# Kernel optimization log

Hardware: AMD Instinct MI355X
Metric: run time of the kernel (lower is better)

The kernel has to match this reference:

```python
import jax, jax.numpy as jnp
import numpy as np
import math

WIN = 2
TOPK = 3
GH, GW = 4, 4  # gabor splatting grid == upsampled window size


def _window_partition(img, ws):
    # img: (B, C, H, W) -> (B, num_windows, ws*ws, C)
    B, C, H, W = img.shape
    x = img.transpose(0, 2, 3, 1)  # B,H,W,C
    x = x.reshape(B, H // ws, ws, W // ws, ws, C)
    x = x.transpose(0, 1, 3, 2, 4, 5).reshape(B, -1, ws * ws, C)
    return x


def _gabor_map(theta, sigma, lam, psi, gamma):
    # build num 4x4 Gabor kernels from per-component params -> (num, GH, GW)
    cy = jnp.arange(GH, dtype=jnp.float32) - (GH - 1) / 2.0
    cx = jnp.arange(GW, dtype=jnp.float32) - (GW - 1) / 2.0
    yy, xx = jnp.meshgrid(cy, cx, indexing='ij')  # (GH, GW)
    th = theta[:, None, None] * (2.0 * jnp.pi)
    xp = xx[None] * jnp.cos(th) + yy[None] * jnp.sin(th)
    yp = -xx[None] * jnp.sin(th) + yy[None] * jnp.cos(th)
    sig = sigma[:, None, None] + 0.5  # keep positive
    lmb = lam[:, None, None] + 0.5
    gam = gamma[:, None, None]
    env = jnp.exp(-(xp ** 2 + (gam ** 2) * yp ** 2) / (2.0 * sig ** 2))
    carrier = jnp.cos(2.0 * jnp.pi * xp / lmb + psi[:, None, None])
    return env * carrier  # (num, GH, GW)


def setup_inputs() -> dict:
    key = jax.random.key(0)
    ks = jax.random.split(key, 8)
    B, Nt, Ns, C = 64, 64, 4096, 256
    return {
        'z': jax.random.normal(ks[0], (B, Nt, C), dtype=jnp.float32),
        'x': jax.random.normal(ks[1], (B, Ns, C), dtype=jnp.float32),
        'gabor_theta': jax.random.uniform(ks[2], (16,), dtype=jnp.float32),
        'gabor_sigma': jax.random.uniform(ks[3], (16,), dtype=jnp.float32),
        'gabor_lam': jax.random.uniform(ks[4], (16,), dtype=jnp.float32),
        'gabor_psi': jax.random.uniform(ks[5], (16,), dtype=jnp.float32),
        'gabor_gamma': jax.random.uniform(ks[6], (16,), dtype=jnp.float32),
        'gabor_weight': jax.random.normal(ks[7], (16,), dtype=jnp.float32),
    }


def reference(z, x, gabor_theta, gabor_sigma, gabor_lam, gabor_psi,
              gabor_gamma, gabor_weight):
    B, Nt, C = z.shape
    ht = int(math.isqrt(Nt))
    _, Ns, _ = x.shape
    hs = int(math.isqrt(Ns))

    z_img = z.transpose(0, 2, 1).reshape(B, C, ht, ht)
    z_max = z_img.max(axis=(2, 3))  # AdaptiveMaxPool2d((1,1)) -> (B, C)

    x_img = x.transpose(0, 2, 1).reshape(B, C, hs, hs)
    x_windows = _window_partition(x_img, WIN)

    # grouped 1x1 xcorr == per-pixel dot product with template vector
    response = jnp.einsum('bchw,bc->bhw', x_img, z_max)[:, None]  # (B,1,hs,hs)
    r_windows = _window_partition(response, WIN)
    win_mean = r_windows.mean(axis=2)[..., 0]  # (B, nW)

    _, idx = jax.lax.top_k(win_mean, TOPK)  # (B, TOPK)
    x_sel = jnp.take_along_axis(x_windows, idx[:, :, None, None], axis=1)
    x_win = x_sel.reshape(B, TOPK, WIN, WIN, C).transpose(0, 1, 4, 2, 3)
    x_win = x_win.reshape(B * TOPK, C, WIN, WIN)

    x_up = jax.image.resize(x_win, (B * TOPK, C, GH, GW), method='bilinear')

    g = _gabor_map(gabor_theta, gabor_sigma, gabor_lam, gabor_psi, gabor_gamma)
    gmap = jnp.einsum('k,khw->hw', gabor_weight, g)  # (GH, GW)
    splat = x_up * gmap  # gabor splatting as multiplicative spatial modulation

    res = (splat + x_up).reshape(B, TOPK, C, GH * GW)
    res = res.transpose(0, 1, 3, 2).reshape(B, TOPK * GH * GW, C)
    return res
```

## Files before the change

kernel.cpp:

```cpp
#include <hip/hip_runtime.h>
#include <math.h>

#define TWO_PI 6.28318530717958647692f


__global__ void k_zmax(const float* __restrict__ z, float* __restrict__ zmax) {
    int b = blockIdx.x;
    int c = threadIdx.x;
    const float* zp = z + (size_t)b * 64 * 256 + c;
    float m = -INFINITY;
#pragma unroll
    for (int n = 0; n < 64; ++n) m = fmaxf(m, zp[n * 256]);
    zmax[b * 256 + c] = m;
}

__global__ void k_resp(const float* __restrict__ x, const float* __restrict__ zmax,
                       float* __restrict__ resp) {
    int blk  = blockIdx.x;
    int b    = blk >> 7;
    int jl   = blk & 127;
    int wave = threadIdx.x >> 6;
    int lane = threadIdx.x & 63;
    float4 zm = ((const float4*)(zmax + b * 256))[lane];
    const float4* xb = (const float4*)(x + (size_t)b * 4096 * 256);
#pragma unroll
    for (int it = 0; it < 8; ++it) {
        int tok = jl * 32 + it * 4 + wave;
        float4 v = xb[(size_t)tok * 64 + lane];
        float d = v.x * zm.x + v.y * zm.y + v.z * zm.z + v.w * zm.w;
#pragma unroll
        for (int off = 32; off > 0; off >>= 1) d += __shfl_down(d, off, 64);
        if (lane == 0) resp[b * 4096 + tok] = d;
    }
}

__global__ void k_topk(const float* __restrict__ resp, int* __restrict__ idxout) {
    __shared__ float wmean[1024];
    __shared__ float rv[256];
    __shared__ int   ri[256];
    int b   = blockIdx.x;
    int tid = threadIdx.x;
    const float* rb = resp + b * 4096;
    for (int widx = tid; widx < 1024; widx += 256) {
        int h0 = (widx >> 5) << 1;
        int w0 = (widx & 31) << 1;
        int base = h0 * 64 + w0;
        float s = rb[base] + rb[base + 1] + rb[base + 64] + rb[base + 65];
        wmean[widx] = s * 0.25f;
    }
    __syncthreads();
    for (int k = 0; k < 3; ++k) {
        float bv = -INFINITY;
        int   bi = 1 << 30;
        for (int widx = tid; widx < 1024; widx += 256) {
            float v = wmean[widx];
            if (v > bv || (v == bv && widx < bi)) { bv = v; bi = widx; }
        }
        rv[tid] = bv; ri[tid] = bi;
        __syncthreads();
        for (int s = 128; s > 0; s >>= 1) {
            if (tid < s) {
                float v2 = rv[tid + s]; int i2 = ri[tid + s];
                if (v2 > rv[tid] || (v2 == rv[tid] && i2 < ri[tid])) { rv[tid] = v2; ri[tid] = i2; }
            }
            __syncthreads();
        }
        if (tid == 0) {
            idxout[b * 3 + k] = ri[0];
            wmean[ri[0]] = -INFINITY;
        }
        __syncthreads();
    }
}

__global__ void k_out(const float* __restrict__ x, const int* __restrict__ idxbuf,
                      const float* __restrict__ theta, const float* __restrict__ sigma,
                      const float* __restrict__ lam,   const float* __restrict__ psi,
                      const float* __restrict__ gamma, const float* __restrict__ wgt,
                      float* __restrict__ out) {
    __shared__ float Xs[4 * 256];
    __shared__ float gm[16];
    int b = blockIdx.x / 3;
    int k = blockIdx.x % 3;
    int tid  = threadIdx.x;
    int tok  = tid >> 6;
    int lane = tid & 63;

    int widx = idxbuf[b * 3 + k];
    int h0 = (widx >> 5) << 1;
    int w0 = (widx & 31) << 1;
    int token_id = (h0 + (tok >> 1)) * 64 + w0 + (tok & 1);
    float4 v = ((const float4*)(x + ((size_t)b * 4096 + token_id) * 256))[lane];
    ((float4*)Xs)[tok * 64 + lane] = v;

    if (tid < 16) {
        int p = tid;
        float yy = (float)(p >> 2) - 1.5f;
        float xx = (float)(p & 3) - 1.5f;
        float acc = 0.0f;
        for (int kk = 0; kk < 16; ++kk) {
            float th = theta[kk] * TWO_PI;
            float sn, cs;
            sincosf(th, &sn, &cs);
            float xp = xx * cs + yy * sn;
            float yp = -xx * sn + yy * cs;
            float sig = sigma[kk] + 0.5f;
            float lmb = lam[kk] + 0.5f;
            float gam = gamma[kk];
            float env = expf(-(xp * xp + gam * gam * yp * yp) / (2.0f * sig * sig));
            float car = cosf(TWO_PI * xp / lmb + psi[kk]);
            acc += wgt[kk] * env * car;
        }
        gm[p] = 1.0f + acc;
    }
    __syncthreads();

    const float WT[4] = {1.0f, 0.75f, 0.25f, 0.0f};
    float4 x00 = ((const float4*)Xs)[0 * 64 + lane];
    float4 x01 = ((const float4*)Xs)[1 * 64 + lane];
    float4 x10 = ((const float4*)Xs)[2 * 64 + lane];
    float4 x11 = ((const float4*)Xs)[3 * 64 + lane];
    float4* ob = (float4*)(out + ((size_t)b * 48 + k * 16) * 256);
#pragma unroll
    for (int it = 0; it < 4; ++it) {
        int p  = it * 4 + (tid >> 6);
        int gy = p >> 2, gx = p & 3;
        float wy0 = WT[gy], wy1 = 1.0f - wy0;
        float wx0 = WT[gx], wx1 = 1.0f - wx0;
        float g = gm[p];
        float4 r;
        r.x = g * (wy0 * (wx0 * x00.x + wx1 * x01.x) + wy1 * (wx0 * x10.x + wx1 * x11.x));
        r.y = g * (wy0 * (wx0 * x00.y + wx1 * x01.y) + wy1 * (wx0 * x10.y + wx1 * x11.y));
        r.z = g * (wy0 * (wx0 * x00.z + wx1 * x01.z) + wy1 * (wx0 * x10.z + wx1 * x11.z));
        r.w = g * (wy0 * (wx0 * x00.w + wx1 * x01.w) + wy1 * (wx0 * x10.w + wx1 * x11.w));
        ob[(size_t)p * 64 + lane] = r;
    }
}

extern "C" void kernel_launch(void* const* d_in, const int* in_sizes, int n_in,
                              void* d_out, int out_size, void* d_ws, size_t ws_size,
                              hipStream_t stream) {
    const float* z     = (const float*)d_in[0];
    const float* x     = (const float*)d_in[1];
    const float* theta = (const float*)d_in[2];
    const float* sigma = (const float*)d_in[3];
    const float* lam   = (const float*)d_in[4];
    const float* psi   = (const float*)d_in[5];
    const float* gamma = (const float*)d_in[6];
    const float* wgt   = (const float*)d_in[7];
    float* out = (float*)d_out;

    float* ws    = (float*)d_ws;
    float* zmax  = ws;
    float* resp  = ws + 16384;
    int*   idxb  = (int*)(ws + 16384 + 262144);

    k_zmax<<<64, 256, 0, stream>>>(z, zmax);
    k_resp<<<8192, 256, 0, stream>>>(x, zmax, resp);
    k_topk<<<64, 256, 0, stream>>>(resp, idxb);
    k_out<<<192, 256, 0, stream>>>(x, idxb, theta, sigma, lam, psi, gamma, wgt, out);
}
```

Measured before the change: 386.4 us.

## Fuse window-mean pooling into response kernel, one wave per 2x2 window

```diff
diff --git a/kernel.cpp b/kernel.cpp
--- a/kernel.cpp
+++ b/kernel.cpp
@@ -14,40 +14,56 @@
     zmax[b * 256 + c] = m;
 }
 
-__global__ void k_resp(const float* __restrict__ x, const float* __restrict__ zmax,
-                       float* __restrict__ resp) {
+__global__ void k_wmean(const float* __restrict__ x, const float* __restrict__ zmax,
+                        float* __restrict__ wmean) {
     int blk  = blockIdx.x;
-    int b    = blk >> 7;
-    int jl   = blk & 127;
+    int b    = blk >> 5;
+    int wh   = blk & 31;
     int wave = threadIdx.x >> 6;
     int lane = threadIdx.x & 63;
-    float4 zm = ((const float4*)(zmax + b * 256))[lane];
+    int g    = lane >> 4;
+    int q    = lane & 15;
+
+    const float4* zm4 = (const float4*)(zmax + b * 256);
+    float4 zm0 = zm4[q];
+    float4 zm1 = zm4[q + 16];
+    float4 zm2 = zm4[q + 32];
+    float4 zm3 = zm4[q + 48];
+
     const float4* xb = (const float4*)(x + (size_t)b * 4096 * 256);
+    int trow = (2 * wh + (g >> 1)) * 64;
+    float* wout = wmean + b * 1024 + wh * 32;
+
 #pragma unroll
-    for (int it = 0; it < 8; ++it) {
-        int tok = jl * 32 + it * 4 + wave;
-        float4 v = xb[(size_t)tok * 64 + lane];
-        float d = v.x * zm.x + v.y * zm.y + v.z * zm.z + v.w * zm.w;
-#pragma unroll
-        for (int off = 32; off > 0; off >>= 1) d += __shfl_down(d, off, 64);
-        if (lane == 0) resp[b * 4096 + tok] = d;
+    for (int p = 0; p < 8; ++p) {
+        int ww  = p * 4 + wave;
+        int tok = trow + 2 * ww + (g & 1);
+        const float4* tp = xb + (size_t)tok * 64;
+        float4 v0 = tp[q];
+        float4 v1 = tp[q + 16];
+        float4 v2 = tp[q + 32];
+        float4 v3 = tp[q + 48];
+        float d = v0.x * zm0.x + v0.y * zm0.y + v0.z * zm0.z + v0.w * zm0.w
+                + v1.x * zm1.x + v1.y * zm1.y + v1.z * zm1.z + v1.w * zm1.w
+                + v2.x * zm2.x + v2.y * zm2.y + v2.z * zm2.z + v2.w * zm2.w
+                + v3.x * zm3.x + v3.y * zm3.y + v3.z * zm3.z + v3.w * zm3.w;
+        d += __shfl_xor(d, 1, 64);
+        d += __shfl_xor(d, 2, 64);
+        d += __shfl_xor(d, 4, 64);
+        d += __shfl_xor(d, 8, 64);
+        d += __shfl_xor(d, 16, 64);
+        d += __shfl_xor(d, 32, 64);
+        if (lane == 0) wout[ww] = d * 0.25f;
     }
 }
 
-__global__ void k_topk(const float* __restrict__ resp, int* __restrict__ idxout) {
+__global__ void k_topk(const float* __restrict__ wmean_g, int* __restrict__ idxout) {
     __shared__ float wmean[1024];
     __shared__ float rv[256];
     __shared__ int   ri[256];
     int b   = blockIdx.x;
     int tid = threadIdx.x;
-    const float* rb = resp + b * 4096;
-    for (int widx = tid; widx < 1024; widx += 256) {
-        int h0 = (widx >> 5) << 1;
-        int w0 = (widx & 31) << 1;
-        int base = h0 * 64 + w0;
-        float s = rb[base] + rb[base + 1] + rb[base + 64] + rb[base + 65];
-        wmean[widx] = s * 0.25f;
-    }
+    for (int widx = tid; widx < 1024; widx += 256) wmean[widx] = wmean_g[b * 1024 + widx];
     __syncthreads();
     for (int k = 0; k < 3; ++k) {
         float bv = -INFINITY;
@@ -152,11 +168,11 @@
 
     float* ws    = (float*)d_ws;
     float* zmax  = ws;
-    float* resp  = ws + 16384;
-    int*   idxb  = (int*)(ws + 16384 + 262144);
+    float* wmean = ws + 16384;
+    int*   idxb  = (int*)(ws + 16384 + 65536);
 
     k_zmax<<<64, 256, 0, stream>>>(z, zmax);
-    k_resp<<<8192, 256, 0, stream>>>(x, zmax, resp);
-    k_topk<<<64, 256, 0, stream>>>(resp, idxb);
+    k_wmean<<<2048, 256, 0, stream>>>(x, zmax, wmean);
+    k_topk<<<64, 256, 0, stream>>>(wmean, idxb);
     k_out<<<192, 256, 0, stream>>>(x, idxb, theta, sigma, lam, psi, gamma, wgt, out);
 }
```

Measured after the change: 384.0 us. About the same (-0.6%).
